# Performance work log

Measured on AMD Instinct MI355X. Metric: run time of the kernel, lower is better.

The kernel has to match this reference:

```python
import jax, jax.numpy as jnp
import numpy as np

jax.config.update("jax_enable_x64", True)  # int64 keys for lattice hashing

_EPS = float(np.finfo(np.float64).eps)
_SIGMA_SPATIAL = 5.0   # spatial stddev (voxels)
_SIGMA_COLOR = 0.25    # intensity stddev
_BASE = 8192           # per-coordinate key range
_OFF = 4096            # coordinate offset so packed keys are non-negative


def _encode(coords):
    """Pack (..., d) integer lattice coords into a single int64 key."""
    enc = jnp.zeros(coords.shape[:-1], jnp.int64)
    for i in range(coords.shape[-1]):
        enc = enc * _BASE + (coords[..., i].astype(jnp.int64) + _OFF)
    return enc


def _bilateral_features(image):
    """Bilateral features: (z,y,x)/sigma_s and intensity/sigma_c. image: (1,D,H,W)."""
    _, D, H, W = image.shape
    z, y, x = jnp.meshgrid(jnp.arange(D, dtype=jnp.float32),
                           jnp.arange(H, dtype=jnp.float32),
                           jnp.arange(W, dtype=jnp.float32), indexing="ij")
    spatial = jnp.stack([z, y, x], -1) / _SIGMA_SPATIAL            # (D,H,W,3)
    color = (image[0] / _SIGMA_COLOR)[..., None]                   # (D,H,W,1)
    return jnp.concatenate([spatial, color], -1).reshape(-1, 4)    # (N,4)


def _permutohedral(q, feats):
    """Permutohedral-lattice Gaussian filtering (splat -> blur -> slice).
    q: (N,C) float32 values, feats: (N,d) float32 positions. Returns (N,C).
    Global scale of the blur kernel cancels in the final normalization."""
    N, d = feats.shape
    dp1 = d + 1
    # ---- elevate features onto the hyperplane H_d ----
    inv_std = np.sqrt(2.0 / 3.0) * dp1
    scale = jnp.asarray([inv_std / np.sqrt((i + 1) * (i + 2)) for i in range(d)], jnp.float32)
    cf = feats * scale
    elev = [None] * dp1
    sm = jnp.zeros((N,), jnp.float32)
    for i in range(d, 0, -1):
        c = cf[:, i - 1]
        elev[i] = sm - i * c
        sm = sm + c
    elev[0] = sm
    elevated = jnp.stack(elev, axis=1)                             # (N, d+1)
    # ---- closest remainder-0 lattice point ----
    rd = jnp.round(elevated / dp1)
    rem0 = rd * dp1
    sum_rd = jnp.sum(rd, axis=1).astype(jnp.int32)
    # ---- rank of each coordinate (ties broken by index) ----
    diff = elevated - rem0
    di = diff[:, :, None]
    dj = diff[:, None, :]
    jlt = (jnp.arange(dp1)[None, :] < jnp.arange(dp1)[:, None])[None]  # mask[i,j] = j < i
    rank = jnp.sum((dj > di) | ((dj == di) & jlt), axis=2).astype(jnp.int32)
    rank = rank + sum_rd[:, None]
    low, high = rank < 0, rank > d
    rank = rank + jnp.where(low, dp1, 0) - jnp.where(high, dp1, 0)
    rem0 = rem0 + jnp.where(low, float(dp1), 0.0) - jnp.where(high, float(dp1), 0.0)
    # ---- barycentric coordinates inside the enclosing simplex ----
    v = (elevated - rem0) / dp1
    rows = jnp.arange(N)[:, None]
    bary = jnp.zeros((N, d + 2), jnp.float32)
    bary = bary.at[rows, d - rank].add(v)
    bary = bary.at[rows, dp1 - rank].add(-v)
    bary = bary.at[:, 0].add(1.0 + bary[:, dp1])
    bary = bary[:, :dp1]                                           # (N, d+1) weights per remainder
    # ---- integer keys of the d+1 simplex vertices (first d coords suffice) ----
    rem0i = rem0[:, :d].astype(jnp.int32)
    keys = jnp.stack([rem0i + jnp.where(rank[:, :d] < dp1 - r, r, r - dp1).astype(jnp.int32)
                      for r in range(dp1)], axis=1)                # (N, d+1, d)
    enc = _encode(keys).reshape(-1)
    Mpad = N * dp1
    sentinel = _BASE ** d                                          # > any real key; sorts last
    uniq, inv = jnp.unique(enc, return_inverse=True, size=Mpad, fill_value=sentinel)
    inv = inv.reshape(N, dp1)
    # ---- splat ----
    C = q.shape[1]
    vals = jnp.zeros((Mpad, C), jnp.float32).at[inv].add(bary[:, :, None] * q[:, None, :])
    # ---- blur along each of the d+1 lattice directions ----
    coords = jnp.stack([(uniq // (_BASE ** (d - 1 - i))) % _BASE - _OFF for i in range(d)],
                       axis=-1).astype(jnp.int32)                  # (Mpad, d)

    def lookup(c):
        e = _encode(c)
        pos = jnp.clip(jnp.searchsorted(uniq, e), 0, Mpad - 1)
        return pos, uniq[pos] == e

    for j in range(dp1):
        off = jnp.ones((d,), jnp.int32)
        if j < d:
            off = off.at[j].set(-d)
        p1, f1 = lookup(coords + off)
        p2, f2 = lookup(coords - off)
        n1 = jnp.where(f1[:, None], vals[p1], 0.0)
        n2 = jnp.where(f2[:, None], vals[p2], 0.0)
        vals = 0.5 * vals + 0.25 * (n1 + n2)
    # ---- slice ----
    return jnp.sum(bary[:, :, None] * vals[inv], axis=1)           # (N, C)


def setup_inputs():
    key = jax.random.key(0)
    k1, k2 = jax.random.split(key)
    input_ = jax.random.uniform(k1, (4, 96, 96, 96), dtype=jnp.float32)
    image = jax.random.uniform(k2, (1, 96, 96, 96), dtype=jnp.float32)
    return {"input_": input_, "image": image}


def reference(input_, image):
    feats = _bilateral_features(image)
    C, D, H, W = input_.shape
    q = input_.reshape(C, -1).T                                    # (N, C)
    ones = jnp.ones((q.shape[0], 1), jnp.float32)                  # fused normalization pass
    filt = _permutohedral(jnp.concatenate([q, ones], axis=1), feats)
    out = filt[:, :C] / (filt[:, C:] + _EPS)                       # == permuto(q) * 1/(permuto(1)+eps)
    return out.T.reshape(C, D, H, W)
```

## Files before the change

### kernel.cpp

```cpp
#include <hip/hip_runtime.h>
#include <hip/hip_fp16.h>
#include <stdint.h>

#define NPTS (96*96*96)
#define NP5  (NPTS*5)

#define GD1 33
#define GD2 29
#define GD3 25
#define GO0 5
#define GO1 16
#define GO2 18
#define GO3 19
#define GS3 5
#define GS2 (GD3*GS3)
#define GS1 (GD2*GS2)
#define GS0 (GD1*GS1)
#define GCELLS (31*GS0)
#define GCELLS1 (GCELLS+1)
#define GSSUM (GS0+GS1+GS2+GS3)

#define LHS 2048

struct LatPt { int cell[5]; float w[5]; };


#define LATTICE_MATH(n)                                                        \
  int x = n % 96, y = (n / 96) % 96, z = n / (96 * 96);                        \
  float cf[4];                                                                 \
  cf[0] = ((float)z / 5.0f) * 2.8867513459481287f;                             \
  cf[1] = ((float)y / 5.0f) * 1.6666666666666667f;                             \
  cf[2] = ((float)x / 5.0f) * 1.1785113019775793f;                             \
  cf[3] = (imgv / 0.25f) * 0.9128709291752769f;                                \
  float elev[5];                                                               \
  float sm = 0.f;                                                              \
  _Pragma("unroll")                                                            \
  for (int i = 4; i >= 1; --i){ float c = cf[i-1]; elev[i] = sm - (float)i * c; sm += c; } \
  elev[0] = sm;                                                                \
  float rem0[5]; float sumrd_f = 0.f;                                          \
  _Pragma("unroll")                                                            \
  for (int i = 0; i < 5; i++){ float rd = rintf(elev[i] / 5.0f); rem0[i] = rd * 5.0f; sumrd_f += rd; } \
  int sum_rd = (int)sumrd_f;                                                   \
  float diff[5];                                                               \
  _Pragma("unroll")                                                            \
  for (int i = 0; i < 5; i++) diff[i] = elev[i] - rem0[i];                     \
  int rank[5];                                                                 \
  _Pragma("unroll")                                                            \
  for (int i = 0; i < 5; i++){                                                 \
    int r = 0;                                                                 \
    _Pragma("unroll")                                                          \
    for (int j = 0; j < 5; j++){                                               \
      r += (diff[j] > diff[i] || (diff[j] == diff[i] && j < i)) ? 1 : 0;       \
    }                                                                          \
    rank[i] = r + sum_rd;                                                      \
  }                                                                            \
  _Pragma("unroll")                                                            \
  for (int i = 0; i < 5; i++){                                                 \
    if (rank[i] < 0)      { rank[i] += 5; rem0[i] += 5.0f; }                   \
    else if (rank[i] > 4) { rank[i] -= 5; rem0[i] -= 5.0f; }                   \
  }                                                                            \
  float b[6] = {0.f,0.f,0.f,0.f,0.f,0.f};                                      \
  _Pragma("unroll")                                                            \
  for (int i = 0; i < 5; i++){                                                 \
    float v = (elev[i] - rem0[i]) / 5.0f;                                      \
    b[4 - rank[i]] += v;                                                       \
    b[5 - rank[i]] -= v;                                                       \
  }                                                                            \
  b[0] += 1.0f + b[5];                                                         \
  int rem0i[4];                                                                \
  _Pragma("unroll")                                                            \
  for (int i = 0; i < 4; i++) rem0i[i] = (int)rem0[i];

__device__ __forceinline__ LatPt lat_compute(int n, float imgv)
{
  LATTICE_MATH(n)
  LatPt p;
  #pragma unroll
  for (int r = 0; r < 5; r++){
    int q0 = (rem0i[0] / 5) - (rank[0] < 5 - r ? 0 : 1) + GO0;
    int q1 = (rem0i[1] / 5) - (rank[1] < 5 - r ? 0 : 1) + GO1;
    int q2 = (rem0i[2] / 5) - (rank[2] < 5 - r ? 0 : 1) + GO2;
    int q3 = (rem0i[3] / 5) - (rank[3] < 5 - r ? 0 : 1) + GO3;
    int cell = (((q0 * GD1 + q1) * GD2 + q2) * GD3 + q3) * 5 + r;
    if ((unsigned)cell >= (unsigned)GCELLS) cell = GCELLS;
    p.cell[r] = cell;
    p.w[r] = b[r];
  }
  return p;
}

__global__ void k_build_hyb(const float* __restrict__ image,
                            const float* __restrict__ input_,
                            int* __restrict__ head,
                            int4* __restrict__ nodes)
{
  __shared__ int   ls_cell[LHS];
  __shared__ int   ls_head[LHS];
  __shared__ short ls_next[1280];
  __shared__ float ls_w[1280];
  __shared__ float ls_q[256 * 4];
  __shared__ short ls_slot[1280];
  __shared__ int   ls_cnt;

  int tid = threadIdx.x;
  #pragma unroll
  for (int i = 0; i < LHS / 256; i++){
    ls_cell[tid + 256 * i] = -1;
    ls_head[tid + 256 * i] = -1;
  }
  if (tid == 0) ls_cnt = 0;
  __syncthreads();

  int n = blockIdx.x * 256 + tid;
  float q0 = input_[n], q1 = input_[NPTS + n], q2 = input_[2 * NPTS + n], q3 = input_[3 * NPTS + n];
  *reinterpret_cast<float4*>(&ls_q[tid * 4]) = make_float4(q0, q1, q2, q3);
  LatPt P = lat_compute(n, image[n]);

  #pragma unroll
  for (int r = 0; r < 5; r++){
    int cell = P.cell[r];
    unsigned int h = ((unsigned int)cell * 2654435761u) & (LHS - 1);
    while (true){
      int prev = atomicCAS(&ls_cell[h], -1, cell);
      if (prev == -1){
        int li = atomicAdd(&ls_cnt, 1);
        ls_slot[li] = (short)h;
        break;
      }
      if (prev == cell) break;
      h = (h + 1) & (LHS - 1);
    }
    int e = tid * 5 + r;
    ls_w[e] = P.w[r];
    ls_next[e] = (short)atomicExch(&ls_head[h], e);
  }
  __syncthreads();

  int cnt = ls_cnt;
  int blockBase = blockIdx.x * 1280;
  for (int i = tid; i < cnt; i += 256){
    int slot = ls_slot[i];
    int cell = ls_cell[slot];
    float s0 = 0.f, s1 = 0.f, s2 = 0.f, s3 = 0.f, s4 = 0.f;
    int e = ls_head[slot];
    while (e >= 0){
      int en = ls_next[e];
      float w = ls_w[e];
      float4 q = *reinterpret_cast<const float4*>(&ls_q[(e / 5) * 4]);
      s0 += w * q.x; s1 += w * q.y; s2 += w * q.z; s3 += w * q.w; s4 += w;
      e = en;
    }
    int node = blockBase + i;
    int old = atomicExch(&head[cell], node);
    __half2 h01 = __floats2half2_rn(s0, s1);
    __half2 h23 = __floats2half2_rn(s2, s3);
    int4 raw;
    raw.x = old;
    raw.y = *reinterpret_cast<int*>(&h01);
    raw.z = *reinterpret_cast<int*>(&h23);
    raw.w = __float_as_int(s4);
    nodes[node] = raw;
  }
}

__global__ void k_gather_agg(const int* __restrict__ head,
                             const int4* __restrict__ nodes,
                             int3* __restrict__ vals,
                             unsigned int* __restrict__ bitmap)
{
  int c = blockIdx.x * blockDim.x + threadIdx.x;
  int e = -1;
  if (c < GCELLS1) e = head[c];
  bool occ = (e >= 0);
  unsigned long long mask = __ballot(occ);
  int lane = threadIdx.x & 63;
  if (lane == 0)       bitmap[c >> 5] = (unsigned int)(mask & 0xffffffffu);
  else if (lane == 32) bitmap[c >> 5] = (unsigned int)(mask >> 32);
  if (c >= GCELLS1) return;

  float s0 = 0.f, s1 = 0.f, s2 = 0.f, s3 = 0.f, s4 = 0.f;
  while (e >= 0){
    int4 raw = nodes[e];
    __half2 h01 = *reinterpret_cast<__half2*>(&raw.y);
    __half2 h23 = *reinterpret_cast<__half2*>(&raw.z);
    float2 f01 = __half22float2(h01);
    float2 f23 = __half22float2(h23);
    s0 += f01.x; s1 += f01.y; s2 += f23.x; s3 += f23.y;
    s4 += __int_as_float(raw.w);
    e = raw.x;
  }
  __half2 o01 = __floats2half2_rn(s0, s1);
  __half2 o23 = __floats2half2_rn(s2, s3);
  int3 rec;
  rec.x = *reinterpret_cast<int*>(&o01);
  rec.y = *reinterpret_cast<int*>(&o23);
  rec.z = __float_as_int(s4);
  vals[c] = rec;
}

__global__ void k_blur_d(const unsigned int* __restrict__ bitmap,
                         const int3* __restrict__ vin,
                         int3* __restrict__ vout,
                         int dPa, int dPb, int dMa, int dMb, int zfill)
{
  int c = blockIdx.x * blockDim.x + threadIdx.x;
  if (c >= GCELLS) return;
  unsigned int w = bitmap[c >> 5];
  if (!((w >> (c & 31)) & 1u)){
    if (zfill){
      int3 zero; zero.x = 0; zero.y = 0; zero.z = 0;
      vout[c] = zero;
    }
    return;
  }
  int r = c % 5;
  int p1 = c + (r == 4 ? dPb : dPa);
  int p2 = c + (r == 0 ? dMb : dMa);
  int3 a  = vin[c];
  int3 b1 = vin[p1];
  int3 b2 = vin[p2];

  float2 a01 = __half22float2(*reinterpret_cast<__half2*>(&a.x));
  float2 a23 = __half22float2(*reinterpret_cast<__half2*>(&a.y));
  float  aw  = __int_as_float(a.z);
  float2 m01 = __half22float2(*reinterpret_cast<__half2*>(&b1.x));
  float2 m23 = __half22float2(*reinterpret_cast<__half2*>(&b1.y));
  float  mw  = __int_as_float(b1.z);
  float2 n01 = __half22float2(*reinterpret_cast<__half2*>(&b2.x));
  float2 n23 = __half22float2(*reinterpret_cast<__half2*>(&b2.y));
  float  nw  = __int_as_float(b2.z);

  float o0 = 0.5f * a01.x + 0.25f * (m01.x + n01.x);
  float o1 = 0.5f * a01.y + 0.25f * (m01.y + n01.y);
  float o2 = 0.5f * a23.x + 0.25f * (m23.x + n23.x);
  float o3 = 0.5f * a23.y + 0.25f * (m23.y + n23.y);
  float ow = 0.5f * aw    + 0.25f * (mw    + nw);

  __half2 o01 = __floats2half2_rn(o0, o1);
  __half2 o23 = __floats2half2_rn(o2, o3);
  int3 rec;
  rec.x = *reinterpret_cast<int*>(&o01);
  rec.y = *reinterpret_cast<int*>(&o23);
  rec.z = __float_as_int(ow);
  vout[c] = rec;
}

__global__ void k_slice_d(const float* __restrict__ image,
                          const int3* __restrict__ vals,
                          float* __restrict__ out)
{
  int n = blockIdx.x * blockDim.x + threadIdx.x;
  if (n >= NPTS) return;
  LatPt P = lat_compute(n, image[n]);

  float s0 = 0.f, s1 = 0.f, s2 = 0.f, s3 = 0.f, s4 = 0.f;
  #pragma unroll
  for (int r = 0; r < 5; r++){
    float w = P.w[r];
    int3 rec = vals[P.cell[r]];
    float2 f01 = __half22float2(*reinterpret_cast<__half2*>(&rec.x));
    float2 f23 = __half22float2(*reinterpret_cast<__half2*>(&rec.y));
    s0 += w * f01.x; s1 += w * f01.y; s2 += w * f23.x; s3 += w * f23.y;
    s4 += w * __int_as_float(rec.z);
  }
  float denom = s4 + 2.2204460492503131e-16f;
  out[n]            = s0 / denom;
  out[NPTS + n]     = s1 / denom;
  out[2 * NPTS + n] = s2 / denom;
  out[3 * NPTS + n] = s3 / denom;
}


extern "C" void kernel_launch(void* const* d_in, const int* in_sizes, int n_in,
                              void* d_out, int out_size, void* d_ws, size_t ws_size,
                              hipStream_t stream)
{
  const float* input_ = (const float*)d_in[0];
  const float* image  = (const float*)d_in[1];
  float* out = (float*)d_out;
  char* ws = (char*)d_ws;

  const int NB = (NPTS + 255) / 256;
  const int CB = (GCELLS1 + 255) / 256;
  const size_t BMWORDS = (size_t)CB * 8;
  const int Sj[5] = { GS0, GS1, GS2, GS3, 0 };

  size_t o = 0;
  size_t off_bm   = o; o += BMWORDS * 4;              o = (o + 255) & ~(size_t)255;
  size_t off_dead = o;
  size_t off_head = o; o += (size_t)GCELLS1 * 4;      o = (o + 255) & ~(size_t)255;
  size_t off_node = o; o += (size_t)NP5 * 16;         o = (o + 255) & ~(size_t)255;
  size_t dead_end = o;
  size_t off_vA   = o; o += (size_t)GCELLS1 * 12;
  size_t vB_need  = (size_t)GCELLS1 * 12;
  size_t off_vB   = off_dead;
  if (dead_end - off_dead < vB_need || o > ws_size){
    off_vB = (o + 255) & ~(size_t)255;
  }

  unsigned int* bitmap = (unsigned int*)(ws + off_bm);
  int*          head   = (int*)(ws + off_head);
  int4*         nodes  = (int4*)(ws + off_node);
  int3*         valsA  = (int3*)(ws + off_vA);
  int3*         valsB  = (int3*)(ws + off_vB);

  hipMemsetAsync(head, 0xFF, (size_t)GCELLS1 * 4, stream);

  k_build_hyb<<<NB, 256, 0, stream>>>(image, input_, head, nodes);
  k_gather_agg<<<CB, 256, 0, stream>>>(head, nodes, valsA, bitmap);

  int3* vin = valsA; int3* vout = valsB;
  for (int j = 0; j < 5; j++){
    int dPa = 1 - Sj[j];
    int dPb = GSSUM - Sj[j] - 4;
    int dMa = Sj[j] - 1;
    int dMb = Sj[j] - GSSUM + 4;
    k_blur_d<<<CB, 256, 0, stream>>>(bitmap, vin, vout, dPa, dPb, dMa, dMb,
                                     (j == 0) ? 1 : 0);
    int3* t = vin; vin = vout; vout = t;
  }

  k_slice_d<<<NB, 256, 0, stream>>>(image, vin, out);
}
```

Before: 183.3 us.

## Fuse pairs of lattice blur passes into single kernels with recomputation

Merges two consecutive blur directions into one kernel. Each thread recomputes the first-direction blur at itself and at its two second-direction neighbours, then applies the second blur. This cuts the five blur launches to three and removes two intermediate full-array write/read round trips. In exchange each output does about three times the first-pass gathers (9 random reads instead of 3), and the intermediate values skip the fp16 rounding step.

```diff
diff --git a/kernel.cpp b/kernel.cpp
--- a/kernel.cpp
+++ b/kernel.cpp
@@ -23,6 +23,7 @@
 #define LHS 2048
 
 struct LatPt { int cell[5]; float w[5]; };
+struct V5 { float s0, s1, s2, s3, w; };
 
 
 #define LATTICE_MATH(n)                                                        \
@@ -198,10 +199,38 @@
   vals[c] = rec;
 }
 
-__global__ void k_blur_d(const unsigned int* __restrict__ bitmap,
-                         const int3* __restrict__ vin,
-                         int3* __restrict__ vout,
-                         int dPa, int dPb, int dMa, int dMb, int zfill)
+__device__ __forceinline__ V5 ublur(const unsigned int* __restrict__ bitmap,
+                                    const int3* __restrict__ vin,
+                                    int d, int dPa, int dPb, int dMa, int dMb)
+{
+  V5 u = {0.f, 0.f, 0.f, 0.f, 0.f};
+  unsigned int wd = bitmap[d >> 5];
+  if (!((wd >> (d & 31)) & 1u)) return u;
+  int rd = d % 5;
+  int p1 = d + (rd == 4 ? dPb : dPa);
+  int p2 = d + (rd == 0 ? dMb : dMa);
+  int3 a  = vin[d];
+  int3 b1 = vin[p1];
+  int3 b2 = vin[p2];
+  float2 a01 = __half22float2(*reinterpret_cast<__half2*>(&a.x));
+  float2 a23 = __half22float2(*reinterpret_cast<__half2*>(&a.y));
+  float2 m01 = __half22float2(*reinterpret_cast<__half2*>(&b1.x));
+  float2 m23 = __half22float2(*reinterpret_cast<__half2*>(&b1.y));
+  float2 n01 = __half22float2(*reinterpret_cast<__half2*>(&b2.x));
+  float2 n23 = __half22float2(*reinterpret_cast<__half2*>(&b2.y));
+  u.s0 = 0.5f * a01.x + 0.25f * (m01.x + n01.x);
+  u.s1 = 0.5f * a01.y + 0.25f * (m01.y + n01.y);
+  u.s2 = 0.5f * a23.x + 0.25f * (m23.x + n23.x);
+  u.s3 = 0.5f * a23.y + 0.25f * (m23.y + n23.y);
+  u.w  = 0.5f * __int_as_float(a.z) + 0.25f * (__int_as_float(b1.z) + __int_as_float(b2.z));
+  return u;
+}
+
+__global__ void k_blur2_d(const unsigned int* __restrict__ bitmap,
+                          const int3* __restrict__ vin,
+                          int3* __restrict__ vout,
+                          int dPaA, int dPbA, int dMaA, int dMbA,
+                          int dPaB, int dPbB, int dMaB, int dMbB, int zfill)
 {
   int c = blockIdx.x * blockDim.x + threadIdx.x;
   if (c >= GCELLS) return;
@@ -214,27 +243,18 @@
     return;
   }
   int r = c % 5;
-  int p1 = c + (r == 4 ? dPb : dPa);
-  int p2 = c + (r == 0 ? dMb : dMa);
-  int3 a  = vin[c];
-  int3 b1 = vin[p1];
-  int3 b2 = vin[p2];
-
-  float2 a01 = __half22float2(*reinterpret_cast<__half2*>(&a.x));
-  float2 a23 = __half22float2(*reinterpret_cast<__half2*>(&a.y));
-  float  aw  = __int_as_float(a.z);
-  float2 m01 = __half22float2(*reinterpret_cast<__half2*>(&b1.x));
-  float2 m23 = __half22float2(*reinterpret_cast<__half2*>(&b1.y));
-  float  mw  = __int_as_float(b1.z);
-  float2 n01 = __half22float2(*reinterpret_cast<__half2*>(&b2.x));
-  float2 n23 = __half22float2(*reinterpret_cast<__half2*>(&b2.y));
-  float  nw  = __int_as_float(b2.z);
-
-  float o0 = 0.5f * a01.x + 0.25f * (m01.x + n01.x);
-  float o1 = 0.5f * a01.y + 0.25f * (m01.y + n01.y);
-  float o2 = 0.5f * a23.x + 0.25f * (m23.x + n23.x);
-  float o3 = 0.5f * a23.y + 0.25f * (m23.y + n23.y);
-  float ow = 0.5f * aw    + 0.25f * (mw    + nw);
+  int q1 = c + (r == 4 ? dPbB : dPaB);
+  int q2 = c + (r == 0 ? dMbB : dMaB);
+
+  V5 uc = ublur(bitmap, vin, c,  dPaA, dPbA, dMaA, dMbA);
+  V5 u1 = ublur(bitmap, vin, q1, dPaA, dPbA, dMaA, dMbA);
+  V5 u2 = ublur(bitmap, vin, q2, dPaA, dPbA, dMaA, dMbA);
+
+  float o0 = 0.5f * uc.s0 + 0.25f * (u1.s0 + u2.s0);
+  float o1 = 0.5f * uc.s1 + 0.25f * (u1.s1 + u2.s1);
+  float o2 = 0.5f * uc.s2 + 0.25f * (u1.s2 + u2.s2);
+  float o3 = 0.5f * uc.s3 + 0.25f * (u1.s3 + u2.s3);
+  float ow = 0.5f * uc.w  + 0.25f * (u1.w  + u2.w);
 
   __half2 o01 = __floats2half2_rn(o0, o1);
   __half2 o23 = __floats2half2_rn(o2, o3);
@@ -242,6 +262,31 @@
   rec.x = *reinterpret_cast<int*>(&o01);
   rec.y = *reinterpret_cast<int*>(&o23);
   rec.z = __float_as_int(ow);
+  vout[c] = rec;
+}
+
+__global__ void k_blur_d(const unsigned int* __restrict__ bitmap,
+                         const int3* __restrict__ vin,
+                         int3* __restrict__ vout,
+                         int dPa, int dPb, int dMa, int dMb, int zfill)
+{
+  int c = blockIdx.x * blockDim.x + threadIdx.x;
+  if (c >= GCELLS) return;
+  unsigned int w = bitmap[c >> 5];
+  if (!((w >> (c & 31)) & 1u)){
+    if (zfill){
+      int3 zero; zero.x = 0; zero.y = 0; zero.z = 0;
+      vout[c] = zero;
+    }
+    return;
+  }
+  V5 u = ublur(bitmap, vin, c, dPa, dPb, dMa, dMb);
+  __half2 o01 = __floats2half2_rn(u.s0, u.s1);
+  __half2 o23 = __floats2half2_rn(u.s2, u.s3);
+  int3 rec;
+  rec.x = *reinterpret_cast<int*>(&o01);
+  rec.y = *reinterpret_cast<int*>(&o23);
+  rec.z = __float_as_int(u.w);
   vout[c] = rec;
 }
 
@@ -284,6 +329,13 @@
   const int CB = (GCELLS1 + 255) / 256;
   const size_t BMWORDS = (size_t)CB * 8;
   const int Sj[5] = { GS0, GS1, GS2, GS3, 0 };
+  int dPa[5], dPb[5], dMa[5], dMb[5];
+  for (int j = 0; j < 5; j++){
+    dPa[j] = 1 - Sj[j];
+    dPb[j] = GSSUM - Sj[j] - 4;
+    dMa[j] = Sj[j] - 1;
+    dMb[j] = Sj[j] - GSSUM + 4;
+  }
 
   size_t o = 0;
   size_t off_bm   = o; o += BMWORDS * 4;              o = (o + 255) & ~(size_t)255;
@@ -309,16 +361,14 @@
   k_build_hyb<<<NB, 256, 0, stream>>>(image, input_, head, nodes);
   k_gather_agg<<<CB, 256, 0, stream>>>(head, nodes, valsA, bitmap);
 
-  int3* vin = valsA; int3* vout = valsB;
-  for (int j = 0; j < 5; j++){
-    int dPa = 1 - Sj[j];
-    int dPb = GSSUM - Sj[j] - 4;
-    int dMa = Sj[j] - 1;
-    int dMb = Sj[j] - GSSUM + 4;
-    k_blur_d<<<CB, 256, 0, stream>>>(bitmap, vin, vout, dPa, dPb, dMa, dMb,
-                                     (j == 0) ? 1 : 0);
-    int3* t = vin; vin = vout; vout = t;
-  }
-
-  k_slice_d<<<NB, 256, 0, stream>>>(image, vin, out);
-}
+  k_blur2_d<<<CB, 256, 0, stream>>>(bitmap, valsA, valsB,
+                                    dPa[0], dPb[0], dMa[0], dMb[0],
+                                    dPa[1], dPb[1], dMa[1], dMb[1], 1);
+  k_blur2_d<<<CB, 256, 0, stream>>>(bitmap, valsB, valsA,
+                                    dPa[2], dPb[2], dMa[2], dMb[2],
+                                    dPa[3], dPb[3], dMa[3], dMb[3], 0);
+  k_blur_d<<<CB, 256, 0, stream>>>(bitmap, valsA, valsB,
+                                   dPa[4], dPb[4], dMa[4], dMb[4], 0);
+
+  k_slice_d<<<NB, 256, 0, stream>>>(image, valsB, out);
+}
```

Result: faster. 175.3 us (-4.4%).
